# Optimization experiments

Measured on AMD Instinct MI355X. Metric: run time of the kernel, lower is better.

Reference implementation:

```python
import jax, jax.numpy as jnp
import numpy as np

SR = 44100
LOWEST = 82.0
L_ORDER = 5
NUM_COEFF = L_ORDER + 1          # 6
NUM_ACTIVE = NUM_COEFF + 1       # 7 (linear interp)
K = int(SR // LOWEST) + NUM_ACTIVE  # coeff_vector_size = 544
N_FRAMES = 100
EXC_FRAMES = 100
EXC_ORDER = 5
BURST_LEN = 2048
N_SAMPLES = 44100


def upsample_linear(frames, T):
    """Linear interpolation of (F,) or (F, C) control frames to T samples (align_corners)."""
    F_ = frames.shape[0]
    pos = jnp.linspace(0.0, F_ - 1.0, T)
    i0 = jnp.clip(jnp.floor(pos).astype(jnp.int32), 0, F_ - 2)
    w = pos - i0.astype(pos.dtype)
    lo = frames[i0]
    hi = frames[i0 + 1]
    if frames.ndim == 2:
        w = w[:, None]
    return lo + (hi - lo) * w


def sample_wise_lpc(x, A):
    """Time-varying all-pole filter: y[t] = x[t] - sum_k A[t,k] * y[t-k-1].
    x: (T,), A: (T, N) -> y: (T,)"""
    N = A.shape[1]

    def step(buf, inp):
        xt, at = inp
        y = xt - jnp.dot(at, buf)  # buf[0]=y[t-1], ..., buf[N-1]=y[t-N]
        buf = jnp.concatenate([y[None], buf[:-1]])
        return buf, y

    _, y = jax.lax.scan(step, jnp.zeros((N,), x.dtype), (x, A))
    return y


def _forward(delay_len_frames, excitation, raw_coeff_frames, raw_gain, exc_coefficients, n_samples):
    T = n_samples
    # --- upsample control signals to audio rate ---
    delay = upsample_linear(delay_len_frames, T)                     # (T,)
    gain = jax.nn.sigmoid(raw_gain) * 0.1 + 0.9
    sb = jax.nn.sigmoid(raw_coeff_frames)                            # (F, 6)
    coeff_frames = sb / sb.sum(axis=-1, keepdims=True) * gain        # normalized, stable
    b = upsample_linear(coeff_frames, T)                             # (T, 6)

    # --- build sparse banded A (linear fractional-delay interpolation) ---
    z_l = jnp.floor(delay).astype(jnp.int32)                         # integer delay
    alfa = delay - z_l.astype(delay.dtype)                           # fractional part
    v0 = -(1.0 - alfa) * b[:, 0]                                     # (T,)
    vmid = -(alfa[:, None] * b[:, :-1] + (1.0 - alfa)[:, None] * b[:, 1:])  # (T, 5)
    vlast = -alfa * b[:, -1]                                         # (T,)
    vals = jnp.concatenate([v0[:, None], vmid, vlast[:, None]], axis=1)     # (T, 7)
    idxs = z_l[:, None] + jnp.arange(NUM_ACTIVE)[None, :]            # (T, 7)
    A = jnp.zeros((T, K), delay.dtype).at[jnp.arange(T)[:, None], idxs].set(vals)

    # --- excitation shaping filter (requires_grad branch) ---
    burst = excitation                                               # (BURST_LEN,)
    a_exc = upsample_linear(exc_coefficients, burst.shape[0])        # (BURST_LEN, 5)
    filtered_burst = sample_wise_lpc(burst, a_exc)

    # --- Karplus-Strong loop: time-varying all-pole with banded A ---
    x = jnp.zeros((T,), burst.dtype).at[: burst.shape[0]].set(filtered_burst)
    y = sample_wise_lpc(x, A)
    return y.astype(jnp.float32)


def setup_inputs() -> dict:
    key = jax.random.key(0)
    k0, k1, k2, k3 = jax.random.split(key, 4)
    # delay in [100, 520] samples so floor(delay)+NUM_ACTIVE-1 < K = 544
    delay_len_frames = 100.0 + 420.0 * jax.random.uniform(k0, (N_FRAMES,), dtype=jnp.float32)
    excitation = jax.random.normal(k1, (BURST_LEN,), dtype=jnp.float32)
    raw_coeff_frames = jax.random.uniform(k2, (N_FRAMES, NUM_COEFF), dtype=jnp.float32,
                                          minval=-2.0, maxval=0.0)
    raw_gain = jnp.asarray(0.0, dtype=jnp.float32)
    exc_coefficients = 0.01 * jax.random.normal(k3, (EXC_FRAMES, EXC_ORDER), dtype=jnp.float32)
    return {
        "delay_len_frames": delay_len_frames,
        "excitation": excitation,
        "raw_coeff_frames": raw_coeff_frames,
        "raw_gain": raw_gain,
        "exc_coefficients": exc_coefficients,
        "n_samples": N_SAMPLES,
    }


def reference(delay_len_frames, excitation, raw_coeff_frames, raw_gain, exc_coefficients, n_samples):
    return _forward(delay_len_frames, excitation, raw_coeff_frames, raw_gain,
                    exc_coefficients, n_samples)
```

## Files before the change

kernel.cpp:

```cpp
#include <hip/hip_runtime.h>
#include <math.h>


#define T_SAMPLES 44100
#define NFRAMES   100
#define NCOEF     6
#define BURST     2048
#define EXC_ORD   5

#define HISTSZ    1096
#define GRPF      9600
#define CFBUF     9856

#define WS_COEF_FLOATS (T_SAMPLES * 12)
#define WS_EXC_OFF     WS_COEF_FLOATS
#define WS_EXC_FLOATS  (EXC_ORD * BURST)
#define WS_TOTAL_BYTES ((size_t)(WS_COEF_FLOATS + WS_EXC_FLOATS) * 4)

__global__ __launch_bounds__(256) void diffks_precompute(
    const float* __restrict__ delay_frames,
    const float* __restrict__ raw_coeff,
    const float* __restrict__ raw_gain,
    const float* __restrict__ exc_coeff,
    float* __restrict__ ws)
{
    int g = blockIdx.x * 256 + threadIdx.x;
    const float gain = 0.1f / (1.0f + expf(-raw_gain[0])) + 0.9f;

    if (g < T_SAMPLES) {
        const float stepT = 99.0f / (float)(T_SAMPLES - 1);
        float pos = (float)g * stepT;
        int i0 = (int)pos; if (i0 > NFRAMES - 2) i0 = NFRAMES - 2;
        float w = pos - (float)i0;

        float d0 = delay_frames[i0], d1 = delay_frames[i0 + 1];
        float delay = d0 + (d1 - d0) * w;
        int z = (int)delay;
        float alfa = delay - (float)z;

        float b[NCOEF];
        {
            float c0v[NCOEF], c1v[NCOEF];
            float s0 = 0.f, s1 = 0.f;
            #pragma unroll
            for (int j = 0; j < NCOEF; ++j) {
                c0v[j] = 1.0f / (1.0f + expf(-raw_coeff[i0 * NCOEF + j]));
                c1v[j] = 1.0f / (1.0f + expf(-raw_coeff[(i0 + 1) * NCOEF + j]));
                s0 += c0v[j]; s1 += c1v[j];
            }
            float g0 = gain / s0, g1 = gain / s1;
            #pragma unroll
            for (int j = 0; j < NCOEF; ++j) {
                float x0 = c0v[j] * g0, x1 = c1v[j] * g1;
                b[j] = x0 + (x1 - x0) * w;
            }
        }
        float oma = 1.0f - alfa;
        float v0 = -oma * b[0];
        float v1 = -(alfa * b[0] + oma * b[1]);
        float v2 = -(alfa * b[1] + oma * b[2]);
        float v3 = -(alfa * b[2] + oma * b[3]);
        float v4 = -(alfa * b[3] + oma * b[4]);
        float v5 = -(alfa * b[4] + oma * b[5]);
        float v6 = -alfa * b[5];
        float pv0 = -v0, pv1 = -v1, pv2 = -v2, pv3 = -v3;
        float pv4 = -v4, pv5 = -v5, pv6 = -v6;

        int base = g - z - 1;
        int q = base - 6;
        int off = q & 1;
        unsigned b2 = ((unsigned)q) & 1022u;

        float m0, m1, m2, m3, m4, m5, m6, m7;
        if (off) { m0 = 0.f; m1 = pv6; m2 = pv5; m3 = pv4;
                   m4 = pv3; m5 = pv2; m6 = pv1; m7 = pv0; }
        else     { m0 = pv6; m1 = pv5; m2 = pv4; m3 = pv3;
                   m4 = pv2; m5 = pv1; m6 = pv0; m7 = 0.f; }

        float4* o = (float4*)(ws + (size_t)g * 12);
        o[0] = make_float4(m0, m1, m2, m3);
        o[1] = make_float4(m4, m5, m6, m7);
        o[2] = make_float4(__int_as_float((int)b2), 0.f, 0.f, 0.f);
    } else if (g < T_SAMPLES + BURST) {
        int te = g - T_SAMPLES;
        const float stepE = 99.0f / (float)(BURST - 1);
        float pos = (float)te * stepE;
        int i0 = (int)pos; if (i0 > NFRAMES - 2) i0 = NFRAMES - 2;
        float w = pos - (float)i0;
        float* o = ws + WS_EXC_OFF + te * EXC_ORD;
        #pragma unroll
        for (int k = 0; k < EXC_ORD; ++k) {
            float a0 = exc_coeff[i0 * EXC_ORD + k];
            float a1 = exc_coeff[(i0 + 1) * EXC_ORD + k];
            o[k] = a0 + (a1 - a0) * w;
        }
    }
}

__device__ __forceinline__ void gload_lds16(const float* g, float* l) {
    __builtin_amdgcn_global_load_lds(
        (const __attribute__((address_space(1))) unsigned int*)(g),
        (__attribute__((address_space(3))) unsigned int*)(l),
        16, 0, 0);
}

__global__ __launch_bounds__(256, 1) void diffks_serial(
    const float* __restrict__ excitation,
    const float* __restrict__ ws,
    float* __restrict__ out)
{
    __shared__ float s_cf[2][CFBUF];
    __shared__ float s_x[64][33];
    __shared__ float s_a[64][161];
    __shared__ float s_hist[HISTSZ];
    __shared__ float s_tail[64][32];
    __shared__ float s_bound[64][6];

    const int tid  = threadIdx.x;
    const int lane = tid & 63;
    const int wv   = tid >> 6;

    for (int t = tid; t < BURST; t += 256)
        s_x[t >> 5][t & 31] = excitation[t];
    for (int i = 0; i < 8; ++i) {
        int t = tid + i * 256;
        const float* g = ws + WS_EXC_OFF + t * EXC_ORD;
        float* dst = &s_a[t >> 5][(t & 31) * 5];
        dst[0] = g[0]; dst[1] = g[1]; dst[2] = g[2];
        dst[3] = g[3]; dst[4] = g[4];
    }
    for (int i = tid; i < HISTSZ; i += 256) s_hist[i] = 0.0f;
    __syncthreads();

    if (tid < 64) {
        float st[6][5];
        #pragma unroll
        for (int r = 0; r < 6; ++r)
            #pragma unroll
            for (int k = 0; k < 5; ++k) st[r][k] = 0.0f;
        #pragma unroll
        for (int r = 1; r <= 5; ++r) st[r][r - 1] = 1.0f;

        const float* ar = &s_a[lane][0];
        const float* xr = &s_x[lane][0];
        #pragma unroll 8
        for (int i = 0; i < 32; ++i) {
            float a0 = ar[i * 5 + 0], a1 = ar[i * 5 + 1], a2 = ar[i * 5 + 2];
            float a3 = ar[i * 5 + 3], a4 = ar[i * 5 + 4];
            float xv = xr[i];
            #pragma unroll
            for (int r = 0; r < 6; ++r) {
                float acc = (r == 0) ? xv : 0.0f;
                acc = fmaf(-a0, st[r][0], acc);
                acc = fmaf(-a1, st[r][1], acc);
                acc = fmaf(-a2, st[r][2], acc);
                acc = fmaf(-a3, st[r][3], acc);
                acc = fmaf(-a4, st[r][4], acc);
                st[r][4] = st[r][3]; st[r][3] = st[r][2];
                st[r][2] = st[r][1]; st[r][1] = st[r][0];
                st[r][0] = acc;
            }
        }
        #pragma unroll
        for (int r = 0; r < 6; ++r)
            #pragma unroll
            for (int k = 0; k < 5; ++k)
                s_tail[lane][r * 5 + k] = st[r][k];
    }
    __syncthreads();

    if (tid == 0) {
        float Y[5] = {0.f, 0.f, 0.f, 0.f, 0.f};
        for (int l = 0; l < 64; ++l) {
            #pragma unroll
            for (int c = 0; c < 5; ++c) s_bound[l][c] = Y[c];
            float tl[30];
            #pragma unroll
            for (int j = 0; j < 30; ++j) tl[j] = s_tail[l][j];
            float ny[5];
            #pragma unroll
            for (int k = 0; k < 5; ++k) {
                float acc = tl[k];
                #pragma unroll
                for (int c = 1; c <= 5; ++c)
                    acc = fmaf(tl[c * 5 + k], Y[c - 1], acc);
                ny[k] = acc;
            }
            #pragma unroll
            for (int k = 0; k < 5; ++k) Y[k] = ny[k];
        }
    }
    __syncthreads();

    if (tid < 64) {
        float b0 = s_bound[lane][0], b1 = s_bound[lane][1], b2 = s_bound[lane][2];
        float b3 = s_bound[lane][3], b4 = s_bound[lane][4];
        const float* ar = &s_a[lane][0];
        float* xr = &s_x[lane][0];
        #pragma unroll 8
        for (int i = 0; i < 32; ++i) {
            float a0 = ar[i * 5 + 0], a1 = ar[i * 5 + 1], a2 = ar[i * 5 + 2];
            float a3 = ar[i * 5 + 3], a4 = ar[i * 5 + 4];
            float acc = xr[i];
            acc = fmaf(-a0, b0, acc);
            acc = fmaf(-a1, b1, acc);
            acc = fmaf(-a2, b2, acc);
            acc = fmaf(-a3, b3, acc);
            acc = fmaf(-a4, b4, acc);
            b4 = b3; b3 = b2; b2 = b1; b1 = b0; b0 = acc;
            xr[i] = acc;
        }
    }
    __syncthreads();

    const bool lane_act = (lane < 50);
    const unsigned dumpA = 1032u + (unsigned)lane;

    #define STAGE_GRP(gg)                                                      \
    {                                                                          \
        float* dstb = &s_cf[(gg) & 1][0];                                      \
        const float* srcb = ws + (size_t)(gg) * GRPF + lane * 4;               \
        const int nis = ((gg) >= 55) ? 5 : 38;                                 \
        for (int i = 0; i < nis; ++i)                                          \
            gload_lds16(srcb + i * 256, dstb + i * 256);                       \
    }

    float4 p0a0, p0a1, p0b0, p0b1, p1a0, p1a1, p1b0, p1b1;
    float4 p2a0, p2a1, p2b0, p2b1, p3a0, p3a1, p3b0, p3b1;
    unsigned q0A, q0B, q1A, q1B, q2A, q2B, q3A, q3B;
    float x0A, x0B, x1A, x1B, x2A, x2B, x3A, x3B;

    #define PREPJ(J, BB)                                                       \
    {                                                                          \
        int b_ = (BB); if (b_ > 440) b_ = 440;                                 \
        const float* bu_ = &s_cf[(b_ >> 3) & 1][0];                            \
        const int ln_ = (b_ & 7) * 100 + lane;                                 \
        const float4* qA_ = (const float4*)(bu_ + ln_ * 12);                   \
        const float4* qB_ = (const float4*)(bu_ + (ln_ + 50) * 12);            \
        p##J##a0 = qA_[0]; p##J##a1 = qA_[1];                                  \
        q##J##A = (unsigned)__float_as_int(qA_[2].x);                          \
        p##J##b0 = qB_[0]; p##J##b1 = qB_[1];                                  \
        q##J##B = (unsigned)__float_as_int(qB_[2].x);                          \
        const int tA_ = b_ * 100 + lane;                                       \
        const int tB_ = tA_ + 50;                                              \
        x##J##A = (lane_act && tA_ < BURST)                                    \
                      ? s_x[(tA_ >> 5) & 63][tA_ & 31] : 0.0f;                 \
        x##J##B = (lane_act && tB_ < BURST)                                    \
                      ? s_x[(tB_ >> 5) & 63][tB_ & 31] : 0.0f;                 \
    }

    #define PREP4(SS)                                                          \
    {                                                                          \
        const int sb_ = (SS) * 4;                                              \
        PREPJ(0, sb_ + 0) PREPJ(1, sb_ + 1)                                    \
        PREPJ(2, sb_ + 2) PREPJ(3, sb_ + 3)                                    \
    }

    #define CBODY(J, BB)                                                       \
    {                                                                          \
        const int t0_ = (BB) * 100;                                            \
        const int tA_ = t0_ + lane;                                            \
        const int tB_ = tA_ + 50;                                              \
        const float2* wA_ = (const float2*)(s_hist + q##J##A);                 \
        const float2* wB_ = (const float2*)(s_hist + q##J##B);                 \
        const float2 a01_ = wA_[0], a23_ = wA_[1];                             \
        const float2 a45_ = wA_[2], a67_ = wA_[3];                             \
        const float2 b01_ = wB_[0], b23_ = wB_[1];                             \
        const float2 b45_ = wB_[2], b67_ = wB_[3];                             \
        const float4 am0_ = p##J##a0, am1_ = p##J##a1;                         \
        const float4 bm0_ = p##J##b0, bm1_ = p##J##b1;                         \
        float accA = x##J##A, accB = x##J##B;                                  \
        accA = fmaf(am1_.w, a67_.y, accA);  accB = fmaf(bm1_.w, b67_.y, accB); \
        accA = fmaf(am1_.z, a67_.x, accA);  accB = fmaf(bm1_.z, b67_.x, accB); \
        accA = fmaf(am1_.y, a45_.y, accA);  accB = fmaf(bm1_.y, b45_.y, accB); \
        accA = fmaf(am1_.x, a45_.x, accA);  accB = fmaf(bm1_.x, b45_.x, accB); \
        accA = fmaf(am0_.w, a23_.y, accA);  accB = fmaf(bm0_.w, b23_.y, accB); \
        accA = fmaf(am0_.z, a23_.x, accA);  accB = fmaf(bm0_.z, b23_.x, accB); \
        accA = fmaf(am0_.y, a01_.y, accA);  accB = fmaf(bm0_.y, b01_.y, accB); \
        accA = fmaf(am0_.x, a01_.x, accA);  accB = fmaf(bm0_.x, b01_.x, accB); \
        const unsigned pA_ = ((unsigned)tA_) & 1023u;                          \
        const unsigned pB_ = ((unsigned)tB_) & 1023u;                          \
        s_hist[lane_act ? pA_ : dumpA] = accA;                                 \
        s_hist[lane_act ? pB_ : dumpA] = accB;                                 \
        {                                                                      \
            const unsigned pm_ = ((unsigned)t0_) & 1023u;                      \
            if (pm_ >= 924u || pm_ < 6u) {                                     \
                s_hist[(lane_act && pA_ < 6u) ? (pA_ + 1024u) : dumpA] = accA; \
                s_hist[(lane_act && pB_ < 6u) ? (pB_ + 1024u) : dumpA] = accB; \
            }                                                                  \
        }                                                                      \
        if (lane_act) { out[tA_] = accA; out[tB_] = accB; }                    \
        asm volatile("s_waitcnt lgkmcnt(0)" ::: "memory");                     \
        __builtin_amdgcn_sched_barrier(0);                                     \
    }

    #define COMPUTE4(SS)                                                       \
    {                                                                          \
        const int fb_ = (SS) * 4;                                              \
        CBODY(0, fb_ + 0) CBODY(1, fb_ + 1)                                    \
        CBODY(2, fb_ + 2) CBODY(3, fb_ + 3)                                    \
    }

    if (wv == 1) {
        STAGE_GRP(0)
        asm volatile("s_waitcnt vmcnt(0)" ::: "memory");
    }
    __syncthreads();
    if (wv == 0) { PREP4(0) }
    __syncthreads();

    #pragma unroll 1
    for (int ss = 0; ss < 110; ++ss) {
        if (wv == (ss & 3)) { COMPUTE4(ss) }
        if (((ss & 1) == 0) && (ss <= 108) && (wv == ((ss + 2) & 3))) {
            STAGE_GRP((ss >> 1) + 1)
        }
        if (wv == ((ss + 1) & 3)) {
            asm volatile("s_waitcnt vmcnt(0)" ::: "memory");
            PREP4(ss + 1)
        }
        asm volatile("s_waitcnt lgkmcnt(0)\n\ts_barrier" ::: "memory");
    }
    if (wv == 2) { CBODY(0, 440) }

    #undef COMPUTE4
    #undef CBODY
    #undef PREP4
    #undef PREPJ
    #undef STAGE_GRP
}

#define CHUNK_FB  101
#define NCH_FB    ((T_SAMPLES + CHUNK_FB - 1) / CHUNK_FB)
#define HIST_FB   1024

__global__ __launch_bounds__(128) void diffks_fallback(
    const float* __restrict__ delay_frames,
    const float* __restrict__ excitation,
    const float* __restrict__ raw_coeff,
    const float* __restrict__ raw_gain,
    const float* __restrict__ exc_coeff,
    float* __restrict__ out)
{
    __shared__ float s_a[EXC_ORD][BURST];
    __shared__ float s_x[BURST];
    __shared__ float s_hist[HIST_FB];
    __shared__ __align__(16) float s_coef[NFRAMES][8];
    __shared__ float s_delay[NFRAMES];

    const int tid = threadIdx.x;
    const float gain = 0.1f / (1.0f + expf(-raw_gain[0])) + 0.9f;

    for (int i = tid; i < NFRAMES; i += 128) s_delay[i] = delay_frames[i];
    for (int f = tid; f < NFRAMES; f += 128) {
        float sb[NCOEF]; float s = 0.0f;
        #pragma unroll
        for (int j = 0; j < NCOEF; ++j) {
            sb[j] = 1.0f / (1.0f + expf(-raw_coeff[f * NCOEF + j]));
            s += sb[j];
        }
        float inv = gain / s;
        #pragma unroll
        for (int j = 0; j < NCOEF; ++j) s_coef[f][j] = sb[j] * inv;
        s_coef[f][6] = 0.0f; s_coef[f][7] = 0.0f;
    }
    const float stepE = 99.0f / 2047.0f;
    for (int t = tid; t < BURST; t += 128) {
        float pos = (float)t * stepE;
        int i0 = (int)pos; if (i0 > NFRAMES - 2) i0 = NFRAMES - 2;
        float w = pos - (float)i0;
        const float* c0 = exc_coeff + i0 * EXC_ORD;
        #pragma unroll
        for (int k = 0; k < EXC_ORD; ++k) {
            float a0 = c0[k], a1 = c0[k + EXC_ORD];
            s_a[k][t] = a0 + (a1 - a0) * w;
        }
        s_x[t] = excitation[t];
    }
    for (int i = tid; i < HIST_FB; i += 128) s_hist[i] = 0.0f;
    __syncthreads();

    if (tid == 0) {
        float y1 = 0.f, y2 = 0.f, y3 = 0.f, y4 = 0.f, y5 = 0.f;
        #pragma unroll 4
        for (int t = 0; t < BURST; ++t) {
            float p = s_x[t];
            p = fmaf(-s_a[1][t], y2, p);
            p = fmaf(-s_a[2][t], y3, p);
            p = fmaf(-s_a[3][t], y4, p);
            p = fmaf(-s_a[4][t], y5, p);
            float y = fmaf(-s_a[0][t], y1, p);
            s_x[t] = y;
            y5 = y4; y4 = y3; y3 = y2; y2 = y1; y1 = y;
        }
    }
    __syncthreads();

    const float stepT = 99.0f / (float)(T_SAMPLES - 1);
    for (int c = 0; c < NCH_FB; ++c) {
        int t = c * CHUNK_FB + tid;
        if (tid < CHUNK_FB && t < T_SAMPLES) {
            float pos = (float)t * stepT;
            int i0 = (int)pos; if (i0 > NFRAMES - 2) i0 = NFRAMES - 2;
            float w = pos - (float)i0;
            float d0 = s_delay[i0], d1 = s_delay[i0 + 1];
            float delay = d0 + (d1 - d0) * w;
            int z = (int)delay;
            float alfa = delay - (float)z;
            const float4* f0 = reinterpret_cast<const float4*>(s_coef[i0]);
            const float4* f1 = reinterpret_cast<const float4*>(s_coef[i0 + 1]);
            float4 c0a = f0[0], c0b = f0[1];
            float4 c1a = f1[0], c1b = f1[1];
            float b[NCOEF];
            b[0] = c0a.x + (c1a.x - c0a.x) * w;
            b[1] = c0a.y + (c1a.y - c0a.y) * w;
            b[2] = c0a.z + (c1a.z - c0a.z) * w;
            b[3] = c0a.w + (c1a.w - c0a.w) * w;
            b[4] = c0b.x + (c1b.x - c0b.x) * w;
            b[5] = c0b.y + (c1b.y - c0b.y) * w;
            float oma = 1.0f - alfa;
            float v[7];
            v[0] = -oma * b[0];
            #pragma unroll
            for (int j = 1; j <= 5; ++j) v[j] = -(alfa * b[j - 1] + oma * b[j]);
            v[6] = -alfa * b[5];
            float x = (t < BURST) ? s_x[t] : 0.0f;
            int base = t - z - 1;
            float sum = 0.0f;
            #pragma unroll
            for (int j = 0; j < 7; ++j) {
                int idx = base - j;
                float yv = s_hist[idx & (HIST_FB - 1)];
                if (idx < 0) yv = 0.0f;
                sum = fmaf(v[j], yv, sum);
            }
            float y = x - sum;
            s_hist[t & (HIST_FB - 1)] = y;
            out[t] = y;
        }
        __syncthreads();
    }
}

extern "C" void kernel_launch(void* const* d_in, const int* in_sizes, int n_in,
                              void* d_out, int out_size, void* d_ws, size_t ws_size,
                              hipStream_t stream) {
    const float* delay_frames = (const float*)d_in[0];
    const float* excitation   = (const float*)d_in[1];
    const float* raw_coeff    = (const float*)d_in[2];
    const float* raw_gain     = (const float*)d_in[3];
    const float* exc_coeff    = (const float*)d_in[4];
    float* out = (float*)d_out;

    if (ws_size >= WS_TOTAL_BYTES) {
        float* ws = (float*)d_ws;
        int gridA = (T_SAMPLES + BURST + 255) / 256;
        diffks_precompute<<<gridA, 256, 0, stream>>>(delay_frames, raw_coeff,
                                                     raw_gain, exc_coeff, ws);
        diffks_serial<<<1, 256, 0, stream>>>(excitation, ws, out);
    } else {
        diffks_fallback<<<1, 128, 0, stream>>>(delay_frames, excitation,
                                               raw_coeff, raw_gain, exc_coeff, out);
    }
}
```

Baseline: 157.2 us.

## Move output stores off the serial compute wave and precompute LDS write indices

```diff
diff --git a/kernel.cpp b/kernel.cpp
--- a/kernel.cpp
+++ b/kernel.cpp
@@ -228,6 +228,8 @@
     float4 p0a0, p0a1, p0b0, p0b1, p1a0, p1a1, p1b0, p1b1;
     float4 p2a0, p2a1, p2b0, p2b1, p3a0, p3a1, p3b0, p3b1;
     unsigned q0A, q0B, q1A, q1B, q2A, q2B, q3A, q3B;
+    unsigned w0A, w0B, w1A, w1B, w2A, w2B, w3A, w3B;
+    unsigned m0A, m0B, m1A, m1B, m2A, m2B, m3A, m3B;
     float x0A, x0B, x1A, x1B, x2A, x2B, x3A, x3B;
 
     #define PREPJ(J, BB)                                                       \
@@ -247,6 +249,12 @@
                       ? s_x[(tA_ >> 5) & 63][tA_ & 31] : 0.0f;                 \
         x##J##B = (lane_act && tB_ < BURST)                                    \
                       ? s_x[(tB_ >> 5) & 63][tB_ & 31] : 0.0f;                 \
+        const unsigned pA_ = ((unsigned)tA_) & 1023u;                          \
+        const unsigned pB_ = ((unsigned)tB_) & 1023u;                          \
+        w##J##A = lane_act ? pA_ : dumpA;                                      \
+        w##J##B = lane_act ? pB_ : dumpA;                                      \
+        m##J##A = (lane_act && pA_ < 6u) ? (pA_ + 1024u) : dumpA;              \
+        m##J##B = (lane_act && pB_ < 6u) ? (pB_ + 1024u) : dumpA;              \
     }
 
     #define PREP4(SS)                                                          \
@@ -256,50 +264,38 @@
         PREPJ(2, sb_ + 2) PREPJ(3, sb_ + 3)                                    \
     }
 
-    #define CBODY(J, BB)                                                       \
+    #define CBODY(J)                                                           \
     {                                                                          \
-        const int t0_ = (BB) * 100;                                            \
-        const int tA_ = t0_ + lane;                                            \
-        const int tB_ = tA_ + 50;                                              \
         const float2* wA_ = (const float2*)(s_hist + q##J##A);                 \
         const float2* wB_ = (const float2*)(s_hist + q##J##B);                 \
         const float2 a01_ = wA_[0], a23_ = wA_[1];                             \
         const float2 a45_ = wA_[2], a67_ = wA_[3];                             \
         const float2 b01_ = wB_[0], b23_ = wB_[1];                             \
         const float2 b45_ = wB_[2], b67_ = wB_[3];                             \
-        const float4 am0_ = p##J##a0, am1_ = p##J##a1;                         \
-        const float4 bm0_ = p##J##b0, bm1_ = p##J##b1;                         \
         float accA = x##J##A, accB = x##J##B;                                  \
-        accA = fmaf(am1_.w, a67_.y, accA);  accB = fmaf(bm1_.w, b67_.y, accB); \
-        accA = fmaf(am1_.z, a67_.x, accA);  accB = fmaf(bm1_.z, b67_.x, accB); \
-        accA = fmaf(am1_.y, a45_.y, accA);  accB = fmaf(bm1_.y, b45_.y, accB); \
-        accA = fmaf(am1_.x, a45_.x, accA);  accB = fmaf(bm1_.x, b45_.x, accB); \
-        accA = fmaf(am0_.w, a23_.y, accA);  accB = fmaf(bm0_.w, b23_.y, accB); \
-        accA = fmaf(am0_.z, a23_.x, accA);  accB = fmaf(bm0_.z, b23_.x, accB); \
-        accA = fmaf(am0_.y, a01_.y, accA);  accB = fmaf(bm0_.y, b01_.y, accB); \
-        accA = fmaf(am0_.x, a01_.x, accA);  accB = fmaf(bm0_.x, b01_.x, accB); \
-        const unsigned pA_ = ((unsigned)tA_) & 1023u;                          \
-        const unsigned pB_ = ((unsigned)tB_) & 1023u;                          \
-        s_hist[lane_act ? pA_ : dumpA] = accA;                                 \
-        s_hist[lane_act ? pB_ : dumpA] = accB;                                 \
-        {                                                                      \
-            const unsigned pm_ = ((unsigned)t0_) & 1023u;                      \
-            if (pm_ >= 924u || pm_ < 6u) {                                     \
-                s_hist[(lane_act && pA_ < 6u) ? (pA_ + 1024u) : dumpA] = accA; \
-                s_hist[(lane_act && pB_ < 6u) ? (pB_ + 1024u) : dumpA] = accB; \
-            }                                                                  \
-        }                                                                      \
-        if (lane_act) { out[tA_] = accA; out[tB_] = accB; }                    \
-        asm volatile("s_waitcnt lgkmcnt(0)" ::: "memory");                     \
-        __builtin_amdgcn_sched_barrier(0);                                     \
-    }
-
-    #define COMPUTE4(SS)                                                       \
-    {                                                                          \
-        const int fb_ = (SS) * 4;                                              \
-        CBODY(0, fb_ + 0) CBODY(1, fb_ + 1)                                    \
-        CBODY(2, fb_ + 2) CBODY(3, fb_ + 3)                                    \
-    }
+        accA = fmaf(p##J##a1.w, a67_.y, accA);                                 \
+        accB = fmaf(p##J##b1.w, b67_.y, accB);                                 \
+        accA = fmaf(p##J##a1.z, a67_.x, accA);                                 \
+        accB = fmaf(p##J##b1.z, b67_.x, accB);                                 \
+        accA = fmaf(p##J##a1.y, a45_.y, accA);                                 \
+        accB = fmaf(p##J##b1.y, b45_.y, accB);                                 \
+        accA = fmaf(p##J##a1.x, a45_.x, accA);                                 \
+        accB = fmaf(p##J##b1.x, b45_.x, accB);                                 \
+        accA = fmaf(p##J##a0.w, a23_.y, accA);                                 \
+        accB = fmaf(p##J##b0.w, b23_.y, accB);                                 \
+        accA = fmaf(p##J##a0.z, a23_.x, accA);                                 \
+        accB = fmaf(p##J##b0.z, b23_.x, accB);                                 \
+        accA = fmaf(p##J##a0.y, a01_.y, accA);                                 \
+        accB = fmaf(p##J##b0.y, b01_.y, accB);                                 \
+        accA = fmaf(p##J##a0.x, a01_.x, accA);                                 \
+        accB = fmaf(p##J##b0.x, b01_.x, accB);                                 \
+        s_hist[w##J##A] = accA;                                                \
+        s_hist[w##J##B] = accB;                                                \
+        s_hist[m##J##A] = accA;                                                \
+        s_hist[m##J##B] = accB;                                                \
+    }
+
+    #define COMPUTE4() { CBODY(0) CBODY(1) CBODY(2) CBODY(3) }
 
     if (wv == 1) {
         STAGE_GRP(0)
@@ -311,9 +307,21 @@
 
     #pragma unroll 1
     for (int ss = 0; ss < 110; ++ss) {
-        if (wv == (ss & 3)) { COMPUTE4(ss) }
+        if (wv == (ss & 3)) { COMPUTE4() }
         if (((ss & 1) == 0) && (ss <= 108) && (wv == ((ss + 2) & 3))) {
             STAGE_GRP((ss >> 1) + 1)
+        }
+        if ((ss >= 1) && (wv == ((ss + 3) & 3))) {
+            const int t0_ = (ss - 1) * 400;
+            #pragma unroll
+            for (int i = 0; i < 6; ++i) {
+                int t_ = t0_ + i * 64 + lane;
+                out[t_] = s_hist[((unsigned)t_) & 1023u];
+            }
+            {
+                int t_ = t0_ + 384 + lane;
+                if (lane < 16) out[t_] = s_hist[((unsigned)t_) & 1023u];
+            }
         }
         if (wv == ((ss + 1) & 3)) {
             asm volatile("s_waitcnt vmcnt(0)" ::: "memory");
@@ -321,7 +329,14 @@
         }
         asm volatile("s_waitcnt lgkmcnt(0)\n\ts_barrier" ::: "memory");
     }
-    if (wv == 2) { CBODY(0, 440) }
+    if (wv == 2) { CBODY(0) }
+    asm volatile("s_waitcnt lgkmcnt(0)\n\ts_barrier" ::: "memory");
+    {
+        int t_ = 43600 + tid;
+        out[t_] = s_hist[((unsigned)t_) & 1023u];
+        t_ += 256;
+        if (t_ < T_SAMPLES) out[t_] = s_hist[((unsigned)t_) & 1023u];
+    }
 
     #undef COMPUTE4
     #undef CBODY
```

After: 158.2 us. Within noise of the previous version (+0.7%).
